# Kernel tuning notes

Measured on AMD Instinct MI355X. Metric: run time of the kernel, lower is better.

The kernel has to match this reference:

```python
import jax, jax.numpy as jnp
import numpy as np

B, S, D, H = 4, 2048, 1024, 16
HD = D // H


def setup_inputs() -> dict:
    key = jax.random.key(0)
    k1, k2, k3 = jax.random.split(key, 3)
    x = jax.random.normal(k1, (B, S, D), dtype=jnp.float32)
    # xavier-ish scaling for stable softmax
    W_attn = jax.random.normal(k2, (3 * D, D), dtype=jnp.float32) * (1.0 / np.sqrt(2 * D))
    b_attn = jnp.zeros((3 * D,), dtype=jnp.float32)
    W_out = jax.random.normal(k3, (D, D), dtype=jnp.float32) * (1.0 / np.sqrt(D))
    b_out = jnp.zeros((D,), dtype=jnp.float32)
    return {"x": x, "W_attn": W_attn, "b_attn": b_attn, "W_out": W_out, "b_out": b_out}


def reference(x, W_attn, b_attn, W_out, b_out):
    bs, seq, d = x.shape
    # fused QKV projection (torch Linear: y = x @ W.T + b)
    kqv = jnp.einsum("bsd,ed->bse", x, W_attn) + b_attn
    # NOTE: source splits as k, q, v (k first)
    k, q, v = jnp.split(kqv, 3, axis=2)
    # [b, s, h, hd] -> [b, h, s, hd]
    k = k.reshape(bs, seq, H, HD).transpose(0, 2, 1, 3)
    q = q.reshape(bs, seq, H, HD).transpose(0, 2, 1, 3)
    v = v.reshape(bs, seq, H, HD).transpose(0, 2, 1, 3)
    scale = 1.0 / np.sqrt(HD)
    scores = jnp.einsum("bhqd,bhkd->bhqk", q, k) * scale
    attn = jax.nn.softmax(scores, axis=-1)
    y = jnp.einsum("bhqk,bhkd->bhqd", attn, v)
    y = y.transpose(0, 2, 1, 3).reshape(bs, seq, d)
    out = jnp.einsum("bsd,ed->bse", y, W_out) + b_out
    return out
```

## Files before the change

### kernel.cpp

```cpp
#include <hip/hip_runtime.h>

typedef unsigned short u16;
typedef unsigned int u32;
typedef __attribute__((ext_vector_type(2))) u32 u32x2;
typedef __attribute__((ext_vector_type(4))) u32 u32x4;
typedef __attribute__((ext_vector_type(8))) short bf16x8;
typedef __attribute__((ext_vector_type(4))) short bf16x4;
typedef __attribute__((ext_vector_type(4))) float f32x4;

__device__ __forceinline__ u16 f2bf(float f) {
  u32 b = __float_as_uint(f);
  b += 0x7fffu + ((b >> 16) & 1u);
  return (u16)(b >> 16);
}

__device__ __forceinline__ u32 pk2bf(float a, float b) {
#if __has_builtin(__builtin_amdgcn_cvt_pk_bf16_f32)
  return __builtin_bit_cast(u32, __builtin_amdgcn_cvt_pk_bf16_f32(a, b));
#else
  return (u32)f2bf(a) | ((u32)f2bf(b) << 16);
#endif
}

__device__ __forceinline__ bf16x4 mk_bf16x4(u32 lo, u32 hi) {
  u32x2 t;
  t[0] = lo;
  t[1] = hi;
  return __builtin_bit_cast(bf16x4, t);
}

__device__ __forceinline__ float fexp2(float x) {
#if __has_builtin(__builtin_amdgcn_exp2f)
  return __builtin_amdgcn_exp2f(x);
#else
  return exp2f(x);
#endif
}

__device__ __forceinline__ f32x4 mfma16x16x16(bf16x4 a, bf16x4 b, f32x4 c) {
#if __has_builtin(__builtin_amdgcn_mfma_f32_16x16x16bf16_1k)
  return __builtin_amdgcn_mfma_f32_16x16x16bf16_1k(a, b, c, 0, 0, 0);
#elif __has_builtin(__builtin_amdgcn_mfma_f32_16x16x16_bf16)
  return __builtin_amdgcn_mfma_f32_16x16x16_bf16(a, b, c, 0, 0, 0);
#else
  asm volatile("v_mfma_f32_16x16x16_bf16 %0, %1, %2, %0\n\ts_nop 7\n\ts_nop 7"
               : "+v"(c)
               : "v"(a), "v"(b));
  return c;
#endif
}

__device__ __forceinline__ void gload_lds16(const u16* g, u16* l) {
  __builtin_amdgcn_global_load_lds((const __attribute__((address_space(1))) void*)g,
                                   (__attribute__((address_space(3))) void*)l, 16, 0, 0);
}

__global__ __launch_bounds__(256) void cvt_f32_bf16(const float* __restrict__ in,
                                                    u16* __restrict__ out) {
  long i = ((long)blockIdx.x * 256 + threadIdx.x) * 8;
  u32 u[8];
#pragma unroll
  for (int j = 0; j < 8; j++) {
    u32 b = __float_as_uint(in[i + j]);
    u[j] = (b + 0x7fffu + ((b >> 16) & 1u)) >> 16;
  }
  u32x4 o;
  o[0] = u[0] | (u[1] << 16);
  o[1] = u[2] | (u[3] << 16);
  o[2] = u[4] | (u[5] << 16);
  o[3] = u[6] | (u[7] << 16);
  *(u32x4*)(out + i) = o;
}

__device__ __forceinline__ void gemm_core_128(const u16* __restrict__ A,
                                              const u16* __restrict__ B, int K,
                                              int m0, int n0, u16* As, u16* Bs,
                                              f32x4 acc[4][4]) {
  int t = threadIdx.x;
  int lane = t & 63, w = t >> 6;
  int quad = lane >> 4, l16 = lane & 15;
  int wm = (w >> 1) * 64, wn = (w & 1) * 64;
  int lr = lane >> 3, lc = lane & 7;
  int cg = lc ^ lr;
  int swz = l16 & 7;
  for (int k0 = 0; k0 < K; k0 += 64) {
#pragma unroll
    for (int i = 0; i < 4; i++) {
      int r0 = i * 32 + w * 8;
      gload_lds16(&A[(long)(m0 + r0 + lr) * K + k0 + cg * 8], &As[r0 * 64]);
      gload_lds16(&B[(long)(n0 + r0 + lr) * K + k0 + cg * 8], &Bs[r0 * 64]);
    }
    __syncthreads();
#pragma unroll
    for (int ks = 0; ks < 2; ks++) {
      bf16x8 a[4], b[4];
#pragma unroll
      for (int tm = 0; tm < 4; tm++)
        a[tm] = *(const bf16x8*)&As[(wm + tm * 16 + l16) * 64 + ((ks * 4 + quad) ^ swz) * 8];
#pragma unroll
      for (int tn = 0; tn < 4; tn++)
        b[tn] = *(const bf16x8*)&Bs[(wn + tn * 16 + l16) * 64 + ((ks * 4 + quad) ^ swz) * 8];
#pragma unroll
      for (int tm = 0; tm < 4; tm++)
#pragma unroll
        for (int tn = 0; tn < 4; tn++)
          acc[tm][tn] = __builtin_amdgcn_mfma_f32_16x16x32_bf16(a[tm], b[tn],
                                                                acc[tm][tn], 0, 0, 0);
    }
    __syncthreads();
  }
}

#define QSCALE 0.1803368801f
__global__ __launch_bounds__(256) void gemm_qkv(const u16* __restrict__ A,
                                                const u16* __restrict__ B,
                                                const float* __restrict__ bias,
                                                u16* __restrict__ Kg,
                                                u16* __restrict__ Qg,
                                                u16* __restrict__ Vg) {
  __shared__ __align__(16) u16 As[128 * 64];
  __shared__ __align__(16) u16 Bs[128 * 64];
  const int K = 1024;
  int m0 = blockIdx.y * 128, n0 = blockIdx.x * 128;
  f32x4 acc[4][4];
#pragma unroll
  for (int i = 0; i < 4; i++)
#pragma unroll
    for (int j = 0; j < 4; j++) acc[i][j] = (f32x4)0.0f;
  gemm_core_128(A, B, K, m0, n0, As, Bs, acc);

  int t = threadIdx.x, lane = t & 63, w = t >> 6;
  int quad = lane >> 4, l16 = lane & 15;
  int wm = (w >> 1) * 64, wn = (w & 1) * 64;
#pragma unroll
  for (int tn = 0; tn < 4; tn++) {
    int n = n0 + wn + tn * 16 + l16;
    float bv = bias[n];
    int which = n >> 10;
    int h = (n >> 6) & 15, d = n & 63;
#pragma unroll
    for (int tm = 0; tm < 4; tm++) {
      int m = m0 + wm + tm * 16 + quad * 4;
      int b = m >> 11, s = m & 2047;
      long bh = (long)b * 16 + h;
      if (which == 2) {
        u32x2 pk;
        pk[0] = pk2bf(acc[tm][tn][0] + bv, acc[tm][tn][1] + bv);
        pk[1] = pk2bf(acc[tm][tn][2] + bv, acc[tm][tn][3] + bv);
        *(u32x2*)&Vg[(bh * 64 + d) * 2048 + s] = pk;
      } else {
#pragma unroll
        for (int r = 0; r < 4; r++) {
          float v = acc[tm][tn][r] + bv;
          if (which == 0)
            Kg[(bh * 2048 + s + r) * 64 + d] = f2bf(v);
          else
            Qg[(bh * 2048 + s + r) * 64 + d] = f2bf(v * QSCALE);
        }
      }
    }
  }
}

__global__ __launch_bounds__(256) void gemm_out(const u16* __restrict__ A,
                                                const u16* __restrict__ B,
                                                const float* __restrict__ bias,
                                                float* __restrict__ out) {
  __shared__ __align__(16) u16 As[128 * 64];
  __shared__ __align__(16) u16 Bs[128 * 64];
  const int K = 1024, N = 1024;
  int m0 = blockIdx.y * 128, n0 = blockIdx.x * 128;
  f32x4 acc[4][4];
#pragma unroll
  for (int i = 0; i < 4; i++)
#pragma unroll
    for (int j = 0; j < 4; j++) acc[i][j] = (f32x4)0.0f;
  gemm_core_128(A, B, K, m0, n0, As, Bs, acc);

  int t = threadIdx.x, lane = t & 63, w = t >> 6;
  int quad = lane >> 4, l16 = lane & 15;
  int wm = (w >> 1) * 64, wn = (w & 1) * 64;
#pragma unroll
  for (int tn = 0; tn < 4; tn++) {
    int n = n0 + wn + tn * 16 + l16;
    float bv = bias[n];
#pragma unroll
    for (int tm = 0; tm < 4; tm++) {
#pragma unroll
      for (int r = 0; r < 4; r++) {
        int m = m0 + wm + tm * 16 + quad * 4 + r;
        out[(long)m * N + n] = acc[tm][tn][r] + bv;
      }
    }
  }
}

__global__ __launch_bounds__(256, 4) void attn_kernel(const u16* __restrict__ Qg,
                                                      const u16* __restrict__ Kg,
                                                      const u16* __restrict__ Vg,
                                                      u16* __restrict__ Y) {
  __shared__ __align__(16) u16 Ks[2][64 * 64];
  __shared__ __align__(16) u16 Vs[2][64 * 64];
  int t = threadIdx.x, lane = t & 63, w = t >> 6;
  int quad = lane >> 4, l16 = lane & 15;
  int bh = blockIdx.y;
  int q0 = blockIdx.x * 128 + w * 32;
  int lr = lane >> 3, lc = lane & 7, cg = lc ^ lr;
  int swz = l16 & 7;

  bf16x8 qf[2][2];
#pragma unroll
  for (int tq = 0; tq < 2; tq++) {
    const u16* qp = Qg + ((long)bh * 2048 + q0 + tq * 16 + l16) * 64;
    qf[tq][0] = *(const bf16x8*)(qp + quad * 8);
    qf[tq][1] = *(const bf16x8*)(qp + 32 + quad * 8);
  }

  float lsum[2] = {0.0f, 0.0f};
  f32x4 acc[4][2];
#pragma unroll
  for (int dt = 0; dt < 4; dt++)
#pragma unroll
    for (int tq = 0; tq < 2; tq++) acc[dt][tq] = (f32x4)0.0f;

  const u16* Kbase = Kg + ((long)bh * 2048 + lr) * 64 + cg * 8;
  const u16* Vbase = Vg + ((long)bh * 64 + lr) * 2048 + cg * 8;

#pragma unroll
  for (int j = 0; j < 2; j++) {
    int r0 = j * 32 + w * 8;
    gload_lds16(Kbase + (long)r0 * 64, &Ks[0][r0 * 64]);
    gload_lds16(Vbase + (long)r0 * 2048, &Vs[0][r0 * 64]);
  }
  __syncthreads();

  int cur = 0;
  for (int kv0 = 0; kv0 < 2048; kv0 += 64, cur ^= 1) {
    if (kv0 + 64 < 2048) {
      int kn = kv0 + 64;
#pragma unroll
      for (int j = 0; j < 2; j++) {
        int r0 = j * 32 + w * 8;
        gload_lds16(Kbase + (long)(kn + r0) * 64, &Ks[cur ^ 1][r0 * 64]);
        gload_lds16(Vbase + (long)r0 * 2048 + kn, &Vs[cur ^ 1][r0 * 64]);
      }
    }
    const u16* Kc = Ks[cur];
    const u16* Vc = Vs[cur];

    bf16x8 kf[4][2];
#pragma unroll
    for (int tn = 0; tn < 4; tn++)
#pragma unroll
      for (int ks = 0; ks < 2; ks++)
        kf[tn][ks] = *(const bf16x8*)&Kc[(tn * 16 + l16) * 64 + ((ks * 4 + quad) ^ swz) * 8];

    bf16x4 pf[2][4];
#pragma unroll
    for (int tq = 0; tq < 2; tq++) {
      f32x4 s[4];
#pragma unroll
      for (int tn = 0; tn < 4; tn++) s[tn] = (f32x4)0.0f;
#pragma unroll
      for (int ks = 0; ks < 2; ks++)
#pragma unroll
        for (int tn = 0; tn < 4; tn++)
          s[tn] = __builtin_amdgcn_mfma_f32_16x16x32_bf16(kf[tn][ks], qf[tq][ks],
                                                          s[tn], 0, 0, 0);
#pragma unroll
      for (int tn = 0; tn < 4; tn++) {
        float e0 = fexp2(s[tn][0]);
        float e1 = fexp2(s[tn][1]);
        float e2 = fexp2(s[tn][2]);
        float e3 = fexp2(s[tn][3]);
        lsum[tq] += (e0 + e1) + (e2 + e3);
        pf[tq][tn] = mk_bf16x4(pk2bf(e0, e1), pk2bf(e2, e3));
      }
    }

#pragma unroll
    for (int tn = 0; tn < 4; tn++) {
      bf16x4 vf[4];
#pragma unroll
      for (int dt = 0; dt < 4; dt++)
        vf[dt] = *(const bf16x4*)&Vc[(dt * 16 + l16) * 64 +
                                     ((tn * 2 + (quad >> 1)) ^ swz) * 8 + (quad & 1) * 4];
#pragma unroll
      for (int tq = 0; tq < 2; tq++)
#pragma unroll
        for (int dt = 0; dt < 4; dt++)
          acc[dt][tq] = mfma16x16x16(vf[dt], pf[tq][tn], acc[dt][tq]);
    }
    __syncthreads();
  }

#pragma unroll
  for (int tq = 0; tq < 2; tq++) {
    lsum[tq] += __shfl_xor(lsum[tq], 16, 64);
    lsum[tq] += __shfl_xor(lsum[tq], 32, 64);
  }

  int b = bh >> 4, h = bh & 15;
#pragma unroll
  for (int tq = 0; tq < 2; tq++) {
    float inv = 1.0f / lsum[tq];
    long row = (long)b * 2048 + q0 + tq * 16 + l16;
#pragma unroll
    for (int dt = 0; dt < 4; dt++) {
      u32x2 pk;
      pk[0] = pk2bf(acc[dt][tq][0] * inv, acc[dt][tq][1] * inv);
      pk[1] = pk2bf(acc[dt][tq][2] * inv, acc[dt][tq][3] * inv);
      *(u32x2*)&Y[row * 1024 + h * 64 + dt * 16 + quad * 4] = pk;
    }
  }
}

extern "C" void kernel_launch(void* const* d_in, const int* in_sizes, int n_in,
                              void* d_out, int out_size, void* d_ws, size_t ws_size,
                              hipStream_t stream) {
  const float* x = (const float*)d_in[0];
  const float* W_attn = (const float*)d_in[1];
  const float* b_attn = (const float*)d_in[2];
  const float* W_out = (const float*)d_in[3];
  const float* b_out = (const float*)d_in[4];
  float* out = (float*)d_out;

  char* ws = (char*)d_ws;
  u16* xb = (u16*)ws;
  u16* Wab = (u16*)(ws + 16777216);
  u16* Wob = (u16*)(ws + 16777216 + 6291456);
  u16* Kg = (u16*)(ws + 25165824);
  u16* Qg = Kg + 8388608;
  u16* Vg = Qg + 8388608;
  u16* Yb = xb;

  cvt_f32_bf16<<<4096, 256, 0, stream>>>(x, xb);
  cvt_f32_bf16<<<1536, 256, 0, stream>>>(W_attn, Wab);
  cvt_f32_bf16<<<512, 256, 0, stream>>>(W_out, Wob);

  gemm_qkv<<<dim3(24, 64), 256, 0, stream>>>(xb, Wab, b_attn, Kg, Qg, Vg);
  attn_kernel<<<dim3(16, 64), 256, 0, stream>>>(Qg, Kg, Vg, Yb);
  gemm_out<<<dim3(8, 64), 256, 0, stream>>>(Yb, Wob, b_out, out);
}
```

Measured before the change: 291.6 us.

## Triple-buffer K/V tiles with one barrier per step and MFMA row sums

The attention kernel moves from a double-buffered K/V loop with two __syncthreads per tile to a three-stage LDS ring. Each step has a single barrier that waits only on older loads (vmcnt(4)), so the next tile's global-to-LDS copy overlaps compute. The softmax denominator is now accumulated with an extra MFMA against a ones vector instead of scalar adds plus cross-lane shuffles, and s_setprio hints are placed around the MFMA blocks. This raises LDS use and lowers the occupancy target from 4 to 3 blocks per CU, and the hand-written waitcnt counts must match the number of issued loads.

```diff
diff --git a/kernel.cpp b/kernel.cpp
--- a/kernel.cpp
+++ b/kernel.cpp
@@ -195,12 +195,78 @@
   }
 }
 
-__global__ __launch_bounds__(256, 4) void attn_kernel(const u16* __restrict__ Qg,
+#define SYNC_V4                                          \
+  __builtin_amdgcn_sched_barrier(0);                     \
+  asm volatile("s_waitcnt vmcnt(4)" ::: "memory");       \
+  __builtin_amdgcn_s_barrier();                          \
+  __builtin_amdgcn_sched_barrier(0)
+
+#define SYNC_V0                                          \
+  __builtin_amdgcn_sched_barrier(0);                     \
+  asm volatile("s_waitcnt vmcnt(0)" ::: "memory");       \
+  __builtin_amdgcn_s_barrier();                          \
+  __builtin_amdgcn_sched_barrier(0)
+
+#define STAGE_KV(tt, bb)                                                       \
+  do {                                                                         \
+    const u16* kp_ = Kbase + (long)(tt)*4096;                                  \
+    const u16* vp_ = Vbase + (tt)*64;                                          \
+    gload_lds16(kp_ + (w * 8) * 64, &Ks3[bb][(w * 8) * 64]);                   \
+    gload_lds16(kp_ + (w * 8 + 32) * 64, &Ks3[bb][(w * 8 + 32) * 64]);         \
+    gload_lds16(vp_ + (long)(w * 8) * 2048, &Vs3[bb][(w * 8) * 64]);           \
+    gload_lds16(vp_ + (long)(w * 8 + 32) * 2048, &Vs3[bb][(w * 8 + 32) * 64]); \
+  } while (0)
+
+#define COMPUTE(bb)                                                            \
+  do {                                                                         \
+    const u16* Kc_ = Ks3[bb];                                                  \
+    const u16* Vc_ = Vs3[bb];                                                  \
+    bf16x8 kf_[4][2];                                                          \
+    _Pragma("unroll") for (int tn = 0; tn < 4; tn++)                           \
+        _Pragma("unroll") for (int ks = 0; ks < 2; ks++)                       \
+            kf_[tn][ks] = *(const bf16x8*)&Kc_[(tn * 16 + l16) * 64 +          \
+                                               ((ks * 4 + quad) ^ swz) * 8];   \
+    bf16x4 pf_[2][4];                                                          \
+    _Pragma("unroll") for (int tq = 0; tq < 2; tq++) {                         \
+      f32x4 s_[4];                                                             \
+      __builtin_amdgcn_s_setprio(1);                                           \
+      _Pragma("unroll") for (int tn = 0; tn < 4; tn++)                         \
+          s_[tn] = __builtin_amdgcn_mfma_f32_16x16x32_bf16(                    \
+              kf_[tn][0], qf[tq][0], Z, 0, 0, 0);                              \
+      _Pragma("unroll") for (int tn = 0; tn < 4; tn++)                         \
+          s_[tn] = __builtin_amdgcn_mfma_f32_16x16x32_bf16(                    \
+              kf_[tn][1], qf[tq][1], s_[tn], 0, 0, 0);                         \
+      __builtin_amdgcn_s_setprio(0);                                           \
+      _Pragma("unroll") for (int tn = 0; tn < 4; tn++) {                       \
+        float e0 = fexp2(s_[tn][0]);                                           \
+        float e1 = fexp2(s_[tn][1]);                                           \
+        float e2 = fexp2(s_[tn][2]);                                           \
+        float e3 = fexp2(s_[tn][3]);                                           \
+        pf_[tq][tn] = mk_bf16x4(pk2bf(e0, e1), pk2bf(e2, e3));                 \
+      }                                                                        \
+    }                                                                          \
+    __builtin_amdgcn_s_setprio(1);                                             \
+    _Pragma("unroll") for (int tn = 0; tn < 4; tn++) {                         \
+      bf16x4 vf_[4];                                                           \
+      _Pragma("unroll") for (int dt = 0; dt < 4; dt++)                         \
+          vf_[dt] = *(const bf16x4*)&Vc_[(dt * 16 + l16) * 64 +                \
+                                         ((tn * 2 + (quad >> 1)) ^ swz) * 8 +  \
+                                         (quad & 1) * 4];                      \
+      acc_sum[0] = mfma16x16x16(ONES, pf_[0][tn], acc_sum[0]);                 \
+      acc_sum[1] = mfma16x16x16(ONES, pf_[1][tn], acc_sum[1]);                 \
+      _Pragma("unroll") for (int tq = 0; tq < 2; tq++)                         \
+          _Pragma("unroll") for (int dt = 0; dt < 4; dt++)                     \
+              acc[dt][tq] = mfma16x16x16(vf_[dt], pf_[tq][tn], acc[dt][tq]);   \
+    }                                                                          \
+    __builtin_amdgcn_s_setprio(0);                                             \
+  } while (0)
+
+__global__ __launch_bounds__(256, 3) void attn_kernel(const u16* __restrict__ Qg,
                                                       const u16* __restrict__ Kg,
                                                       const u16* __restrict__ Vg,
                                                       u16* __restrict__ Y) {
-  __shared__ __align__(16) u16 Ks[2][64 * 64];
-  __shared__ __align__(16) u16 Vs[2][64 * 64];
+  __shared__ __align__(16) u16 Ks3[3][64 * 64];
+  __shared__ __align__(16) u16 Vs3[3][64 * 64];
   int t = threadIdx.x, lane = t & 63, w = t >> 6;
   int quad = lane >> 4, l16 = lane & 15;
   int bh = blockIdx.y;
@@ -216,94 +282,44 @@
     qf[tq][1] = *(const bf16x8*)(qp + 32 + quad * 8);
   }
 
-  float lsum[2] = {0.0f, 0.0f};
+  const f32x4 Z = {0.0f, 0.0f, 0.0f, 0.0f};
+  const bf16x4 ONES = mk_bf16x4(0x3F803F80u, 0x3F803F80u);
+
   f32x4 acc[4][2];
+  f32x4 acc_sum[2];
 #pragma unroll
   for (int dt = 0; dt < 4; dt++)
 #pragma unroll
     for (int tq = 0; tq < 2; tq++) acc[dt][tq] = (f32x4)0.0f;
+  acc_sum[0] = (f32x4)0.0f;
+  acc_sum[1] = (f32x4)0.0f;
 
   const u16* Kbase = Kg + ((long)bh * 2048 + lr) * 64 + cg * 8;
   const u16* Vbase = Vg + ((long)bh * 64 + lr) * 2048 + cg * 8;
 
-#pragma unroll
-  for (int j = 0; j < 2; j++) {
-    int r0 = j * 32 + w * 8;
-    gload_lds16(Kbase + (long)r0 * 64, &Ks[0][r0 * 64]);
-    gload_lds16(Vbase + (long)r0 * 2048, &Vs[0][r0 * 64]);
-  }
-  __syncthreads();
-
-  int cur = 0;
-  for (int kv0 = 0; kv0 < 2048; kv0 += 64, cur ^= 1) {
-    if (kv0 + 64 < 2048) {
-      int kn = kv0 + 64;
-#pragma unroll
-      for (int j = 0; j < 2; j++) {
-        int r0 = j * 32 + w * 8;
-        gload_lds16(Kbase + (long)(kn + r0) * 64, &Ks[cur ^ 1][r0 * 64]);
-        gload_lds16(Vbase + (long)r0 * 2048 + kn, &Vs[cur ^ 1][r0 * 64]);
-      }
-    }
-    const u16* Kc = Ks[cur];
-    const u16* Vc = Vs[cur];
-
-    bf16x8 kf[4][2];
-#pragma unroll
-    for (int tn = 0; tn < 4; tn++)
-#pragma unroll
-      for (int ks = 0; ks < 2; ks++)
-        kf[tn][ks] = *(const bf16x8*)&Kc[(tn * 16 + l16) * 64 + ((ks * 4 + quad) ^ swz) * 8];
-
-    bf16x4 pf[2][4];
-#pragma unroll
-    for (int tq = 0; tq < 2; tq++) {
-      f32x4 s[4];
-#pragma unroll
-      for (int tn = 0; tn < 4; tn++) s[tn] = (f32x4)0.0f;
-#pragma unroll
-      for (int ks = 0; ks < 2; ks++)
-#pragma unroll
-        for (int tn = 0; tn < 4; tn++)
-          s[tn] = __builtin_amdgcn_mfma_f32_16x16x32_bf16(kf[tn][ks], qf[tq][ks],
-                                                          s[tn], 0, 0, 0);
-#pragma unroll
-      for (int tn = 0; tn < 4; tn++) {
-        float e0 = fexp2(s[tn][0]);
-        float e1 = fexp2(s[tn][1]);
-        float e2 = fexp2(s[tn][2]);
-        float e3 = fexp2(s[tn][3]);
-        lsum[tq] += (e0 + e1) + (e2 + e3);
-        pf[tq][tn] = mk_bf16x4(pk2bf(e0, e1), pk2bf(e2, e3));
-      }
-    }
-
-#pragma unroll
-    for (int tn = 0; tn < 4; tn++) {
-      bf16x4 vf[4];
-#pragma unroll
-      for (int dt = 0; dt < 4; dt++)
-        vf[dt] = *(const bf16x4*)&Vc[(dt * 16 + l16) * 64 +
-                                     ((tn * 2 + (quad >> 1)) ^ swz) * 8 + (quad & 1) * 4];
-#pragma unroll
-      for (int tq = 0; tq < 2; tq++)
-#pragma unroll
-        for (int dt = 0; dt < 4; dt++)
-          acc[dt][tq] = mfma16x16x16(vf[dt], pf[tq][tn], acc[dt][tq]);
-    }
-    __syncthreads();
-  }
-
+  STAGE_KV(0, 0);
+  STAGE_KV(1, 1);
+
+  for (int base = 0; base < 30; base += 3) {
+    SYNC_V4;
+    STAGE_KV(base + 2, 2);
+    COMPUTE(0);
+    SYNC_V4;
+    STAGE_KV(base + 3, 0);
+    COMPUTE(1);
+    SYNC_V4;
+    STAGE_KV(base + 4, 1);
+    COMPUTE(2);
+  }
+  SYNC_V4;
+  COMPUTE(0);
+  SYNC_V0;
+  COMPUTE(1);
+
+  int b = bh >> 4, h = bh & 15;
 #pragma unroll
   for (int tq = 0; tq < 2; tq++) {
-    lsum[tq] += __shfl_xor(lsum[tq], 16, 64);
-    lsum[tq] += __shfl_xor(lsum[tq], 32, 64);
-  }
-
-  int b = bh >> 4, h = bh & 15;
-#pragma unroll
-  for (int tq = 0; tq < 2; tq++) {
-    float inv = 1.0f / lsum[tq];
+    float inv = 1.0f / acc_sum[tq][0];
     long row = (long)b * 2048 + q0 + tq * 16 + l16;
 #pragma unroll
     for (int dt = 0; dt < 4; dt++) {
```

New measurement: 298.1 us. +2.2%, slower.
